# Optimization experiments

Hardware: AMD Instinct MI355X
Metric: run time of the kernel (lower is better)

## Reference

```python
import jax, jax.numpy as jnp
import numpy as np

RADIUS = 5.0
NB = 50                      # num_basis = radius * basis_density_per_A
SN, VN = 16, 8               # node irreps: 16x0e + 8x1o
SO, VO = 8, 4                # out  irreps:  8x0e + 4x1o
H = 128                      # MLP hidden width
NUMEL1 = SN*SN + SN*VN + VN*VN + VN*SN            # 576  (uvw paths, sh muls = 1)
NUMEL2 = SN*SN*SO + SN*VN*VO + VN*SN*VO + VN*VN*SO  # 3584
N_NODES, N_EDGES = 10000, 50000
SQ3 = 3.0 ** 0.5

# normalize2mom constant for silu (e3nn normalizes act so E[act(z)^2]=1, z~N(0,1))
_z = np.linspace(-10.0, 10.0, 40001)
_dz = _z[1] - _z[0]
_phi = np.exp(-0.5 * _z**2) / np.sqrt(2.0 * np.pi)
_s = _z / (1.0 + np.exp(-_z))
ACT_C = float(1.0 / np.sqrt(np.sum(_s * _s * _phi) * _dz))


def _mlp(x, w1, w2):
    # e3nn FullyConnectedNet: variance-preserving layers, normalized act on hidden
    h = ACT_C * jax.nn.silu(x @ (w1 / np.sqrt(w1.shape[0])))
    return h @ (w2 / np.sqrt(w2.shape[0]))


def _soft_one_hot(d):
    # soft_one_hot_linspace(basis='smooth_finite', cutoff=True)
    step = RADIUS / (NB + 1)
    values = jnp.linspace(0.0, RADIUS, NB + 2)[1:-1]
    diff = (d[:, None] - values) / step
    def sus(t):
        return jnp.where(t > 0.0, jnp.exp(-1.0 / jnp.where(t > 0.0, t, 1.0)), 0.0)
    return 1.14136 * np.exp(2.0) * sus(diff + 1.0) * sus(1.0 - diff)


def setup_inputs() -> dict:
    key = jax.random.key(0)
    ks = jax.random.split(key, 7)
    return {
        "edge_index": jax.random.randint(ks[0], (2, N_EDGES), 0, N_NODES),
        "pos": 1.5 * jax.random.normal(ks[1], (N_NODES, 3), jnp.float32),
        "x": jax.random.normal(ks[2], (N_NODES, SN + 3 * VN), jnp.float32),
        "lig_w1": jax.random.normal(ks[3], (NB, H), jnp.float32),
        "lig_w2": jax.random.normal(ks[4], (H, NUMEL1), jnp.float32),
        "rec_w1": jax.random.normal(ks[5], (NB, H), jnp.float32),
        "rec_w2": jax.random.normal(ks[6], (H, NUMEL2), jnp.float32),
    }


def reference(edge_index, pos, x, lig_w1, lig_w2, rec_w1, rec_w2):
    rec, lig = edge_index[0], edge_index[1]
    vec = pos[lig] - pos[rec]                         # [E,3]
    d = jnp.sqrt(jnp.sum(vec * vec, axis=1))
    sh1 = SQ3 * vec / jnp.maximum(d, 1e-12)[:, None]  # l=1 SH, 'component' norm; sh0 == 1
    demb = _soft_one_hot(d) * np.sqrt(NB)             # [E,NB]

    # ---- TP1: node(lig) x sh -> node, per-edge uvw weights ----
    w = _mlp(demb, lig_w1, lig_w2)                    # [E,576]
    o = 0
    W000 = w[:, o:o + SN * SN].reshape(-1, SN, SN); o += SN * SN
    W011 = w[:, o:o + SN * VN].reshape(-1, SN, VN); o += SN * VN
    W101 = w[:, o:o + VN * VN].reshape(-1, VN, VN); o += VN * VN
    W110 = w[:, o:o + VN * SN].reshape(-1, VN, SN)
    xl = x[lig]
    s1 = xl[:, :SN]
    v1 = xl[:, SN:].reshape(-1, VN, 3)
    c0 = (1.0 / (SN + VN)) ** 0.5                     # path norm, out 0e
    c1 = (3.0 / (SN + VN)) ** 0.5                     # path norm, out 1o
    v1_dot_sh = jnp.einsum('euk,ek->eu', v1, sh1)
    s_a = c0 * (jnp.einsum('euw,eu->ew', W000, s1)
                + jnp.einsum('euw,eu->ew', W110, v1_dot_sh) / SQ3)
    v_a = (c1 / SQ3) * (jnp.einsum('euw,eu,ek->ewk', W011, s1, sh1)
                        + jnp.einsum('euw,euk->ewk', W101, v1))

    # ---- TP2: msg x node(rec) -> out, per-edge uvw weights ----
    w = _mlp(demb, rec_w1, rec_w2)                    # [E,3584]
    o = 0
    W000 = w[:, o:o + SN * SN * SO].reshape(-1, SN, SN, SO); o += SN * SN * SO
    W011 = w[:, o:o + SN * VN * VO].reshape(-1, SN, VN, VO); o += SN * VN * VO
    W101 = w[:, o:o + VN * SN * VO].reshape(-1, VN, SN, VO); o += VN * SN * VO
    W110 = w[:, o:o + VN * VN * SO].reshape(-1, VN, VN, SO)
    xr = x[rec]
    s_b = xr[:, :SN]
    v_b = xr[:, SN:].reshape(-1, VN, 3)
    c0 = (1.0 / (SN * SN + VN * VN)) ** 0.5
    c1 = (3.0 / (SN * VN + VN * SN)) ** 0.5
    s_out = c0 * (jnp.einsum('euvw,eu,ev->ew', W000, s_a, s_b)
                  + jnp.einsum('euvw,euk,evk->ew', W110, v_a, v_b) / SQ3)
    v_out = (c1 / SQ3) * (jnp.einsum('euvw,eu,evk->ewk', W011, s_a, v_b)
                          + jnp.einsum('euvw,euk,ev->ewk', W101, v_a, s_b))
    return jnp.concatenate([s_out, v_out.reshape(-1, VO * 3)], axis=1)  # [E, 20]
```

## Files before the change

### kernel.cpp

```cpp
#include <hip/hip_runtime.h>
#include <math.h>

#define NE     50000
#define NNODE  10000
#define HDIM   128
#define GBIN   2048
#define NLUT   2049
#define NC     4160
#define NC1    576
#define NCHMAX 3611
#define MPAD   2064
#define NB_W2T 1040
#define NB_EDGE 196

typedef _Float16 h2 __attribute__((ext_vector_type(2)));
typedef _Float16 h8 __attribute__((ext_vector_type(8)));
typedef float f32x4 __attribute__((ext_vector_type(4)));

typedef __fp16 hp2 __attribute__((ext_vector_type(2)));
typedef __fp16 hp4 __attribute__((ext_vector_type(4)));
typedef __fp16 hp8 __attribute__((ext_vector_type(8)));

static __device__ __forceinline__ float fdot2f(hp2 p, hp2 q, float acc) {
  return __builtin_amdgcn_fdot2(p, q, acc, false);
}
static __device__ __forceinline__ hp2 pk2(float a, float b) {
  hp2 r = __builtin_amdgcn_cvt_pkrtz(a, b);
  return r;
}
static __device__ __forceinline__ hp2 mkh2(__fp16 a, __fp16 b) {
  hp2 o; o[0] = a; o[1] = b;
  return o;
}

#define SQ3C        1.7320508075688772f
#define INV_SQ3     0.5773502691896258f
#define C0_1F       0.20412414523193154f
#define C1_1_OS3F   0.20412414523193154f
#define C0_2F       0.05590169943749474f
#define C1_2_OS3F   0.0625f
#define INV_SQRT_H  0.08838834764831845f
#define DELTA       (5.0f/2048.0f)
#define INV_DELTA   409.6f
#define STEP_INV    (51.0f/5.0f)

__global__ __launch_bounds__(256) void k_fused(
    const float* __restrict__ lw1, const float* __restrict__ rw1,
    const float* __restrict__ lw2, const float* __restrict__ rw2,
    const float actc, const float K0C,
    _Float16* __restrict__ Hl, _Float16* __restrict__ Hr,
    _Float16* __restrict__ w2t,
    const int* __restrict__ ei, const float* __restrict__ pos,
    float* __restrict__ out, int* __restrict__ bin_e,
    float* __restrict__ f_e, int* __restrict__ cnt) {
  const int bid = blockIdx.x;
  const int tid = threadIdx.x;
  if (bid < MPAD) {
    const int g = bid;
    const int which = tid >> 7, hc = tid & 127;
    const float* __restrict__ w1 = which ? rw1 : lw1;
    float h = 0.f;
    if (g <= GBIN) {
      const float tt = (float)g * DELTA * STEP_INV;
      const int i0 = (int)floorf(tt);
      float z = 0.f;
#pragma unroll
      for (int k = 0; k < 2; ++k) {
        const int ii = i0 + k;
        if (ii >= 1 && ii <= 50) {
          const float diff = tt - (float)ii;
          const float a = diff + 1.f, b = 1.f - diff;
          if (a > 0.f && b > 0.f) {
            const float val = K0C * __expf(-1.f / a - 1.f / b);
            z += val * w1[(ii - 1) * HDIM + hc];
          }
        }
      }
      h = actc * z / (1.f + __expf(-z)) * INV_SQRT_H;
    }
    _Float16* __restrict__ H = which ? Hr : Hl;
    H[(size_t)g * HDIM + hc] = (_Float16)h;
  } else if (bid < MPAD + NB_W2T) {
    const int gid = (bid - MPAD) * 256 + tid;
    const int k2 = gid / NC;
    const int n  = gid - k2 * NC;
    float a, b;
    if (n < NC1) {
      a = lw2[(size_t)(2 * k2) * NC1 + n];
      b = lw2[(size_t)(2 * k2 + 1) * NC1 + n];
    } else {
      const int m = n - NC1;
      a = rw2[(size_t)(2 * k2) * 3584 + m];
      b = rw2[(size_t)(2 * k2 + 1) * 3584 + m];
    }
    h2 p; p[0] = (_Float16)a; p[1] = (_Float16)b;
    *(h2*)(w2t + (size_t)n * HDIM + 2 * k2) = p;
  } else {
    const int e = (bid - MPAD - NB_W2T) * 256 + tid;
    if (e >= NE) return;
    const int rec = ei[e], lig = ei[NE + e];
    const float ax = pos[lig * 3 + 0] - pos[rec * 3 + 0];
    const float ay = pos[lig * 3 + 1] - pos[rec * 3 + 1];
    const float az = pos[lig * 3 + 2] - pos[rec * 3 + 2];
    const float d = sqrtf(ax * ax + ay * ay + az * az);
    if (d > 0.f && d < 5.0f) {
      const float tf = d * INV_DELTA;
      int b = (int)tf;
      if (b > GBIN - 1) b = GBIN - 1;
      bin_e[e] = b;
      f_e[e] = tf - (float)b;
      atomicAdd(&cnt[b], 1);
    } else {
      bin_e[e] = -1;
      float* o = out + (size_t)e * 20;
#pragma unroll
      for (int i2 = 0; i2 < 20; ++i2) o[i2] = 0.f;
    }
  }
}

__global__ __launch_bounds__(256) void k_lutm(
    const _Float16* __restrict__ Hl, const _Float16* __restrict__ Hr,
    const _Float16* __restrict__ w2t, _Float16* __restrict__ lut) {
  const int tid = threadIdx.x;
  const int nt = blockIdx.y * 4 + (tid >> 6);
  const int mt = blockIdx.x;
  const int l  = tid & 63;
  const int rc = l & 15;
  const int kg = (l >> 4) * 8;
  const _Float16* __restrict__ Ap =
      ((nt < 36) ? Hl : Hr) + (size_t)(mt * 16 + rc) * HDIM + kg;
  const _Float16* __restrict__ Bp = w2t + (size_t)(nt * 16 + rc) * HDIM + kg;
  f32x4 acc = {0.f, 0.f, 0.f, 0.f};
#pragma unroll
  for (int kc = 0; kc < 4; ++kc) {
    h8 a = *(const h8*)(Ap + kc * 32);
    h8 b = *(const h8*)(Bp + kc * 32);
    acc = __builtin_amdgcn_mfma_f32_16x16x32_f16(a, b, acc, 0, 0, 0);
  }
#pragma unroll
  for (int r = 0; r < 4; ++r) {
    const int g = mt * 16 + (l >> 4) * 4 + r;
    if (g <= GBIN) lut[(size_t)g * NC + nt * 16 + rc] = (_Float16)acc[r];
  }
}

__global__ void k_scan(const int* __restrict__ cnt, int* __restrict__ offs,
                       int* __restrict__ woff, int* __restrict__ chunk_bin,
                       int* __restrict__ chunk_start, int* __restrict__ nch) {
  __shared__ int lds[256];
  const int t = threadIdx.x;
  int loc[8];
  int s = 0;
#pragma unroll
  for (int i = 0; i < 8; ++i) { loc[i] = cnt[t * 8 + i]; s += loc[i]; }
  lds[t] = s;
  __syncthreads();
  for (int o = 1; o < 256; o <<= 1) {
    int v = 0;
    if (t >= o) v = lds[t - o];
    __syncthreads();
    lds[t] += v;
    __syncthreads();
  }
  int run = lds[t] - s;
  int runs[8];
#pragma unroll
  for (int i = 0; i < 8; ++i) {
    runs[i] = run;
    offs[t * 8 + i] = run;
    woff[t * 8 + i] = run;
    run += loc[i];
  }
  if (t == 255) offs[GBIN] = run;

  int ccnt[8];
  int csum = 0;
#pragma unroll
  for (int i = 0; i < 8; ++i) { ccnt[i] = (loc[i] + 31) >> 5; csum += ccnt[i]; }
  __syncthreads();
  lds[t] = csum;
  __syncthreads();
  for (int o = 1; o < 256; o <<= 1) {
    int v = 0;
    if (t >= o) v = lds[t - o];
    __syncthreads();
    lds[t] += v;
    __syncthreads();
  }
  int crun = lds[t] - csum;
#pragma unroll
  for (int i = 0; i < 8; ++i) {
    for (int c = 0; c < ccnt[i]; ++c) {
      chunk_bin[crun]   = t * 8 + i;
      chunk_start[crun] = runs[i] + c * 32;
      ++crun;
    }
  }
  if (t == 255) nch[0] = lds[255];
}

__global__ void k_scatter(const int* __restrict__ bin_e, int* __restrict__ woff,
                          int* __restrict__ sorted) {
  const int e = blockIdx.x * 256 + threadIdx.x;
  if (e >= NE) return;
  const int b = bin_e[e];
  if (b >= 0) {
    const int p = atomicAdd(&woff[b], 1);
    sorted[p] = e;
  }
}

__global__ __launch_bounds__(128) void k_epi(
    const _Float16* __restrict__ lut, const int* __restrict__ chunk_bin,
    const int* __restrict__ chunk_start, const int* __restrict__ offs,
    const int* __restrict__ sorted, const float* __restrict__ f_e,
    const int* __restrict__ ei, const float* __restrict__ pos,
    const float* __restrict__ x, float* __restrict__ out,
    const int* __restrict__ nch) {
  __shared__ __fp16 WP[2 * NC];
  const int bid = blockIdx.x;
  if (bid >= nch[0]) return;
  const int b     = chunk_bin[bid];
  const int start = chunk_start[bid];
  const int end0  = offs[b + 1];
  const int end   = (start + 32 < end0) ? (start + 32) : end0;
  const int tid = threadIdx.x;
  {
    const hp8* r0 = (const hp8*)(lut + (size_t)b * NC);
    const hp8* r1 = (const hp8*)(lut + (size_t)(b + 1) * NC);
    hp8* dst = (hp8*)WP;
    for (int i = tid; i < NC / 8; i += 128) {
      hp8 a = r0[i], c = r1[i];
      dst[2 * i]     = __builtin_shufflevector(a, c, 0, 8, 1, 9, 2, 10, 3, 11);
      dst[2 * i + 1] = __builtin_shufflevector(a, c, 4, 12, 5, 13, 6, 14, 7, 15);
    }
  }
  __syncthreads();
  const int s  = tid & 3;
  const int qb = (tid & 63) & ~3;
  const int slot = start + (tid >> 2);
  if (slot >= end) return;

  const int e = sorted[slot];
  const float f = f_e[e];
  const float fm = 1.f - f;
  const int rec = ei[e], lig = ei[NE + e];
  const float ax = pos[lig * 3 + 0] - pos[rec * 3 + 0];
  const float ay = pos[lig * 3 + 1] - pos[rec * 3 + 1];
  const float az = pos[lig * 3 + 2] - pos[rec * 3 + 2];
  const float d = sqrtf(ax * ax + ay * ay + az * az);
  const float inv = SQ3C / fmaxf(d, 1e-12f);
  const float sh0 = ax * inv, sh1 = ay * inv, sh2 = az * inv;

  float s1[16], v1[24];
  {
    const float4* xl = (const float4*)(x + (size_t)lig * 40);
#pragma unroll
    for (int j = 0; j < 4; ++j) {
      float4 v = xl[j];
      s1[j * 4 + 0] = v.x; s1[j * 4 + 1] = v.y; s1[j * 4 + 2] = v.z; s1[j * 4 + 3] = v.w;
    }
#pragma unroll
    for (int j = 0; j < 6; ++j) {
      float4 v = xl[4 + j];
      v1[j * 4 + 0] = v.x; v1[j * 4 + 1] = v.y; v1[j * 4 + 2] = v.z; v1[j * 4 + 3] = v.w;
    }
  }
  float vs[8];
#pragma unroll
  for (int u = 0; u < 8; ++u)
    vs[u] = (v1[u * 3] * sh0 + v1[u * 3 + 1] * sh1 + v1[u * 3 + 2] * sh2) * INV_SQ3;

  float A[4] = {0.f, 0.f, 0.f, 0.f};
#pragma unroll
  for (int u = 0; u < 16; ++u) {
    hp8 w = *(const hp8*)(WP + 2 * (u * 16 + s * 4));
    hp2 sp = pk2(s1[u] * fm, s1[u] * f);
    A[0] = fdot2f(mkh2(w[0], w[1]), sp, A[0]);
    A[1] = fdot2f(mkh2(w[2], w[3]), sp, A[1]);
    A[2] = fdot2f(mkh2(w[4], w[5]), sp, A[2]);
    A[3] = fdot2f(mkh2(w[6], w[7]), sp, A[3]);
  }
#pragma unroll
  for (int u = 0; u < 8; ++u) {
    hp8 w = *(const hp8*)(WP + 2 * (448 + u * 16 + s * 4));
    hp2 sp = pk2(vs[u] * fm, vs[u] * f);
    A[0] = fdot2f(mkh2(w[0], w[1]), sp, A[0]);
    A[1] = fdot2f(mkh2(w[2], w[3]), sp, A[1]);
    A[2] = fdot2f(mkh2(w[4], w[5]), sp, A[2]);
    A[3] = fdot2f(mkh2(w[6], w[7]), sp, A[3]);
  }
  const float sa0 = C0_1F * A[0];
  const float sa1 = C0_1F * A[1];
  const float sa2 = C0_1F * A[2];
  const float sa3 = C0_1F * A[3];

  float vaA0, vaA1, vaA2, vaB0, vaB1, vaB2;
  {
    float cA = 0.f, cB = 0.f;
#pragma unroll
    for (int u = 0; u < 16; ++u) {
      hp4 w = *(const hp4*)(WP + 2 * (256 + u * 8 + s * 2));
      hp2 sp = pk2(s1[u] * fm, s1[u] * f);
      cA = fdot2f(mkh2(w[0], w[1]), sp, cA);
      cB = fdot2f(mkh2(w[2], w[3]), sp, cB);
    }
    float tAx = 0.f, tAy = 0.f, tAz = 0.f, tBx = 0.f, tBy = 0.f, tBz = 0.f;
#pragma unroll
    for (int u = 0; u < 8; ++u) {
      hp4 w = *(const hp4*)(WP + 2 * (384 + u * 8 + s * 2));
      hp2 px = pk2(v1[u * 3] * fm,     v1[u * 3] * f);
      hp2 py = pk2(v1[u * 3 + 1] * fm, v1[u * 3 + 1] * f);
      hp2 pz = pk2(v1[u * 3 + 2] * fm, v1[u * 3 + 2] * f);
      hp2 pa = mkh2(w[0], w[1]);
      hp2 pb = mkh2(w[2], w[3]);
      tAx = fdot2f(pa, px, tAx); tAy = fdot2f(pa, py, tAy); tAz = fdot2f(pa, pz, tAz);
      tBx = fdot2f(pb, px, tBx); tBy = fdot2f(pb, py, tBy); tBz = fdot2f(pb, pz, tBz);
    }
    vaA0 = C1_1_OS3F * (cA * sh0 + tAx);
    vaA1 = C1_1_OS3F * (cA * sh1 + tAy);
    vaA2 = C1_1_OS3F * (cA * sh2 + tAz);
    vaB0 = C1_1_OS3F * (cB * sh0 + tBx);
    vaB1 = C1_1_OS3F * (cB * sh1 + tBy);
    vaB2 = C1_1_OS3F * (cB * sh2 + tBz);
  }

  float saF[16];
#pragma unroll
  for (int k = 0; k < 16; ++k) {
    const float v = ((k & 3) == 0) ? sa0 : ((k & 3) == 1) ? sa1 : ((k & 3) == 2) ? sa2 : sa3;
    saF[k] = __shfl(v, qb + (k >> 2), 64);
  }
  float vaF[24];
#pragma unroll
  for (int w = 0; w < 8; ++w) {
    const int src = qb + (w >> 1);
    const float x0 = (w & 1) ? vaB0 : vaA0;
    const float x1 = (w & 1) ? vaB1 : vaA1;
    const float x2 = (w & 1) ? vaB2 : vaA2;
    vaF[w * 3 + 0] = __shfl(x0, src, 64);
    vaF[w * 3 + 1] = __shfl(x1, src, 64);
    vaF[w * 3 + 2] = __shfl(x2, src, 64);
  }

  const float* xr = x + (size_t)rec * 40;
  const float sbl0 = xr[s],      sbl1 = xr[4 + s];
  const float sbl2 = xr[8 + s],  sbl3 = xr[12 + s];
  const float vbA0 = xr[16 + s * 3 + 0], vbA1 = xr[16 + s * 3 + 1], vbA2 = xr[16 + s * 3 + 2];
  const float vbB0 = xr[16 + (s + 4) * 3 + 0], vbB1 = xr[16 + (s + 4) * 3 + 1], vbB2 = xr[16 + (s + 4) * 3 + 2];

  float oe[20];

  {
    float so[8];
#pragma unroll
    for (int w = 0; w < 8; ++w) so[w] = 0.f;
#pragma unroll
    for (int u = 0; u < 16; ++u) {
      const float su = saF[u];
      const __fp16* rp = WP + 2 * (576 + u * 128 + s * 8);
#pragma unroll
      for (int vv = 0; vv < 4; ++vv) {
        const float q = su * ((vv == 0) ? sbl0 : (vv == 1) ? sbl1 : (vv == 2) ? sbl2 : sbl3);
        hp2 qp = pk2(q * fm, q * f);
        hp8 wa = *(const hp8*)(rp + 2 * (vv * 32));
        hp8 wb = *(const hp8*)(rp + 2 * (vv * 32) + 8);
        so[0] = fdot2f(mkh2(wa[0], wa[1]), qp, so[0]);
        so[1] = fdot2f(mkh2(wa[2], wa[3]), qp, so[1]);
        so[2] = fdot2f(mkh2(wa[4], wa[5]), qp, so[2]);
        so[3] = fdot2f(mkh2(wa[6], wa[7]), qp, so[3]);
        so[4] = fdot2f(mkh2(wb[0], wb[1]), qp, so[4]);
        so[5] = fdot2f(mkh2(wb[2], wb[3]), qp, so[5]);
        so[6] = fdot2f(mkh2(wb[4], wb[5]), qp, so[6]);
        so[7] = fdot2f(mkh2(wb[6], wb[7]), qp, so[7]);
      }
    }
#pragma unroll
    for (int u = 0; u < 8; ++u) {
      const float a0 = vaF[u * 3], a1 = vaF[u * 3 + 1], a2 = vaF[u * 3 + 2];
      const __fp16* rp = WP + 2 * (3648 + u * 64 + s * 8);
#pragma unroll
      for (int vv = 0; vv < 2; ++vv) {
        const float b0v = vv ? vbB0 : vbA0;
        const float b1v = vv ? vbB1 : vbA1;
        const float b2v = vv ? vbB2 : vbA2;
        const float dd = (a0 * b0v + a1 * b1v + a2 * b2v) * INV_SQ3;
        hp2 qp = pk2(dd * fm, dd * f);
        hp8 wa = *(const hp8*)(rp + 2 * (vv * 32));
        hp8 wb = *(const hp8*)(rp + 2 * (vv * 32) + 8);
        so[0] = fdot2f(mkh2(wa[0], wa[1]), qp, so[0]);
        so[1] = fdot2f(mkh2(wa[2], wa[3]), qp, so[1]);
        so[2] = fdot2f(mkh2(wa[4], wa[5]), qp, so[2]);
        so[3] = fdot2f(mkh2(wa[6], wa[7]), qp, so[3]);
        so[4] = fdot2f(mkh2(wb[0], wb[1]), qp, so[4]);
        so[5] = fdot2f(mkh2(wb[2], wb[3]), qp, so[5]);
        so[6] = fdot2f(mkh2(wb[4], wb[5]), qp, so[6]);
        so[7] = fdot2f(mkh2(wb[6], wb[7]), qp, so[7]);
      }
    }
#pragma unroll
    for (int w = 0; w < 8; ++w) oe[w] = C0_2F * so[w];
  }

  {
    float uo[12];
#pragma unroll
    for (int w = 0; w < 12; ++w) uo[w] = 0.f;
#pragma unroll
    for (int u = 0; u < 16; ++u) {
      const float su = saF[u];
      const __fp16* rp = WP + 2 * (2624 + u * 32 + s * 4);
#pragma unroll
      for (int vv = 0; vv < 2; ++vv) {
        const float q0 = su * (vv ? vbB0 : vbA0);
        const float q1 = su * (vv ? vbB1 : vbA1);
        const float q2 = su * (vv ? vbB2 : vbA2);
        hp2 q0p = pk2(q0 * fm, q0 * f);
        hp2 q1p = pk2(q1 * fm, q1 * f);
        hp2 q2p = pk2(q2 * fm, q2 * f);
        hp8 w = *(const hp8*)(rp + 2 * (vv * 16));
        hp2 p0 = mkh2(w[0], w[1]);
        hp2 p1 = mkh2(w[2], w[3]);
        hp2 p2 = mkh2(w[4], w[5]);
        hp2 p3 = mkh2(w[6], w[7]);
        uo[0] = fdot2f(p0, q0p, uo[0]); uo[1]  = fdot2f(p0, q1p, uo[1]);  uo[2]  = fdot2f(p0, q2p, uo[2]);
        uo[3] = fdot2f(p1, q0p, uo[3]); uo[4]  = fdot2f(p1, q1p, uo[4]);  uo[5]  = fdot2f(p1, q2p, uo[5]);
        uo[6] = fdot2f(p2, q0p, uo[6]); uo[7]  = fdot2f(p2, q1p, uo[7]);  uo[8]  = fdot2f(p2, q2p, uo[8]);
        uo[9] = fdot2f(p3, q0p, uo[9]); uo[10] = fdot2f(p3, q1p, uo[10]); uo[11] = fdot2f(p3, q2p, uo[11]);
      }
    }
#pragma unroll
    for (int u = 0; u < 8; ++u) {
      const float a0 = vaF[u * 3], a1 = vaF[u * 3 + 1], a2 = vaF[u * 3 + 2];
      const __fp16* rp = WP + 2 * (3136 + u * 64 + s * 4);
#pragma unroll
      for (int vv = 0; vv < 4; ++vv) {
        const float sbv = (vv == 0) ? sbl0 : (vv == 1) ? sbl1 : (vv == 2) ? sbl2 : sbl3;
        const float q0 = a0 * sbv, q1 = a1 * sbv, q2 = a2 * sbv;
        hp2 q0p = pk2(q0 * fm, q0 * f);
        hp2 q1p = pk2(q1 * fm, q1 * f);
        hp2 q2p = pk2(q2 * fm, q2 * f);
        hp8 w = *(const hp8*)(rp + 2 * (vv * 16));
        hp2 p0 = mkh2(w[0], w[1]);
        hp2 p1 = mkh2(w[2], w[3]);
        hp2 p2 = mkh2(w[4], w[5]);
        hp2 p3 = mkh2(w[6], w[7]);
        uo[0] = fdot2f(p0, q0p, uo[0]); uo[1]  = fdot2f(p0, q1p, uo[1]);  uo[2]  = fdot2f(p0, q2p, uo[2]);
        uo[3] = fdot2f(p1, q0p, uo[3]); uo[4]  = fdot2f(p1, q1p, uo[4]);  uo[5]  = fdot2f(p1, q2p, uo[5]);
        uo[6] = fdot2f(p2, q0p, uo[6]); uo[7]  = fdot2f(p2, q1p, uo[7]);  uo[8]  = fdot2f(p2, q2p, uo[8]);
        uo[9] = fdot2f(p3, q0p, uo[9]); uo[10] = fdot2f(p3, q1p, uo[10]); uo[11] = fdot2f(p3, q2p, uo[11]);
      }
    }
#pragma unroll
    for (int w = 0; w < 12; ++w) oe[8 + w] = C1_2_OS3F * uo[w];
  }

#pragma unroll
  for (int w = 0; w < 20; ++w) {
    oe[w] += __shfl_xor(oe[w], 1, 64);
    oe[w] += __shfl_xor(oe[w], 2, 64);
  }
  if (s == 0) {
    float4* op = (float4*)(out + (size_t)e * 20);
#pragma unroll
    for (int j = 0; j < 5; ++j) {
      float4 o4;
      o4.x = oe[j * 4 + 0]; o4.y = oe[j * 4 + 1];
      o4.z = oe[j * 4 + 2]; o4.w = oe[j * 4 + 3];
      op[j] = o4;
    }
  }
}

extern "C" void kernel_launch(void* const* d_in, const int* in_sizes, int n_in,
                              void* d_out, int out_size, void* d_ws, size_t ws_size,
                              hipStream_t stream) {
  const int*   ei  = (const int*)d_in[0];
  const float* pos = (const float*)d_in[1];
  const float* x   = (const float*)d_in[2];
  const float* lw1 = (const float*)d_in[3];
  const float* lw2 = (const float*)d_in[4];
  const float* rw1 = (const float*)d_in[5];
  const float* rw2 = (const float*)d_in[6];
  float* out = (float*)d_out;
  char*  ws  = (char*)d_ws;

  size_t o = 0;
  _Float16* lut = (_Float16*)(ws + o); o += (size_t)NLUT * NC * 2;
  o = (o + 15) & ~(size_t)15;
  _Float16* Hl  = (_Float16*)(ws + o); o += (size_t)MPAD * HDIM * 2;
  _Float16* Hr  = (_Float16*)(ws + o); o += (size_t)MPAD * HDIM * 2;
  _Float16* w2t = (_Float16*)(ws + o); o += (size_t)NC * HDIM * 2;
  o = (o + 15) & ~(size_t)15;
  int*   bin_e = (int*)(ws + o);  o += (size_t)NE * 4;
  float* f_e   = (float*)(ws + o); o += (size_t)NE * 4;
  int*   cnt   = (int*)(ws + o);  o += (size_t)GBIN * 4;
  int*   offs  = (int*)(ws + o);  o += (size_t)(GBIN + 1) * 4 + 12;
  int*   woff  = (int*)(ws + o);  o += (size_t)GBIN * 4;
  int*   sorted = (int*)(ws + o); o += (size_t)NE * 4;
  int*   chunk_bin   = (int*)(ws + o); o += (size_t)NCHMAX * 4;
  int*   chunk_start = (int*)(ws + o); o += (size_t)NCHMAX * 4;
  int*   nch = (int*)(ws + o); o += 16;

  double ssum = 0.0;
  const double dz = 20.0 / 40000.0;
  for (int i = 0; i <= 40000; ++i) {
    const double z = -10.0 + dz * (double)i;
    const double sil = z / (1.0 + exp(-z));
    const double phi = exp(-0.5 * z * z) / sqrt(2.0 * M_PI);
    ssum += sil * sil * phi;
  }
  const float actc = (float)(1.0 / sqrt(ssum * dz));
  const float k0c  = (float)(1.14136 * exp(2.0));

  hipMemsetAsync(cnt, 0, GBIN * 4, stream);
  k_fused<<<MPAD + NB_W2T + NB_EDGE, 256, 0, stream>>>(
      lw1, rw1, lw2, rw2, actc, k0c, Hl, Hr, w2t, ei, pos, out, bin_e, f_e, cnt);
  k_lutm<<<dim3(129, 65), 256, 0, stream>>>(Hl, Hr, w2t, lut);
  k_scan<<<1, 256, 0, stream>>>(cnt, offs, woff, chunk_bin, chunk_start, nch);
  k_scatter<<<(NE + 255) / 256, 256, 0, stream>>>(bin_e, woff, sorted);
  k_epi<<<NCHMAX, 128, 0, stream>>>(lut, chunk_bin, chunk_start, offs, sorted, f_e,
                                    ei, pos, x, out, nch);
}
```

Measured before the change: 107.0 us.

## Store LUT pre-interleaved by adjacent bins and fold scan into GEMM launch

The LUT GEMM now writes each value twice into an interleaved layout that pairs bin g with bin g+1. The epilogue can then fill its shared-memory table with a straight vector copy instead of loading two rows and shuffling them. The single-block scan kernel becomes one extra block of the GEMM grid, which removes a launch. In exchange the LUT roughly doubles in size, the GEMM writes scattered 2-byte strided stores, and the scan block is serialized inside a large grid.

```diff
diff --git a/kernel.cpp b/kernel.cpp
--- a/kernel.cpp
+++ b/kernel.cpp
@@ -5,13 +5,13 @@
 #define NNODE  10000
 #define HDIM   128
 #define GBIN   2048
-#define NLUT   2049
 #define NC     4160
 #define NC1    576
 #define NCHMAX 3611
 #define MPAD   2064
 #define NB_W2T 1040
 #define NB_EDGE 196
+#define NB_GEMM (129*65)
 
 typedef _Float16 h2 __attribute__((ext_vector_type(2)));
 typedef _Float16 h8 __attribute__((ext_vector_type(8)));
@@ -121,83 +121,90 @@
 
 __global__ __launch_bounds__(256) void k_lutm(
     const _Float16* __restrict__ Hl, const _Float16* __restrict__ Hr,
-    const _Float16* __restrict__ w2t, _Float16* __restrict__ lut) {
+    const _Float16* __restrict__ w2t, __fp16* __restrict__ ilut,
+    const int* __restrict__ cnt, int* __restrict__ offs,
+    int* __restrict__ woff, int* __restrict__ chunk_bin,
+    int* __restrict__ chunk_start, int* __restrict__ nch) {
+  const int bid = blockIdx.x;
   const int tid = threadIdx.x;
-  const int nt = blockIdx.y * 4 + (tid >> 6);
-  const int mt = blockIdx.x;
-  const int l  = tid & 63;
-  const int rc = l & 15;
-  const int kg = (l >> 4) * 8;
-  const _Float16* __restrict__ Ap =
-      ((nt < 36) ? Hl : Hr) + (size_t)(mt * 16 + rc) * HDIM + kg;
-  const _Float16* __restrict__ Bp = w2t + (size_t)(nt * 16 + rc) * HDIM + kg;
-  f32x4 acc = {0.f, 0.f, 0.f, 0.f};
-#pragma unroll
-  for (int kc = 0; kc < 4; ++kc) {
-    h8 a = *(const h8*)(Ap + kc * 32);
-    h8 b = *(const h8*)(Bp + kc * 32);
-    acc = __builtin_amdgcn_mfma_f32_16x16x32_f16(a, b, acc, 0, 0, 0);
-  }
-#pragma unroll
-  for (int r = 0; r < 4; ++r) {
-    const int g = mt * 16 + (l >> 4) * 4 + r;
-    if (g <= GBIN) lut[(size_t)g * NC + nt * 16 + rc] = (_Float16)acc[r];
-  }
-}
-
-__global__ void k_scan(const int* __restrict__ cnt, int* __restrict__ offs,
-                       int* __restrict__ woff, int* __restrict__ chunk_bin,
-                       int* __restrict__ chunk_start, int* __restrict__ nch) {
-  __shared__ int lds[256];
-  const int t = threadIdx.x;
-  int loc[8];
-  int s = 0;
-#pragma unroll
-  for (int i = 0; i < 8; ++i) { loc[i] = cnt[t * 8 + i]; s += loc[i]; }
-  lds[t] = s;
-  __syncthreads();
-  for (int o = 1; o < 256; o <<= 1) {
-    int v = 0;
-    if (t >= o) v = lds[t - o];
+  if (bid < NB_GEMM) {
+    const int mt = bid % 129;
+    const int nt = (bid / 129) * 4 + (tid >> 6);
+    const int l  = tid & 63;
+    const int rc = l & 15;
+    const int kg = (l >> 4) * 8;
+    const _Float16* __restrict__ Ap =
+        ((nt < 36) ? Hl : Hr) + (size_t)(mt * 16 + rc) * HDIM + kg;
+    const _Float16* __restrict__ Bp = w2t + (size_t)(nt * 16 + rc) * HDIM + kg;
+    f32x4 acc = {0.f, 0.f, 0.f, 0.f};
+#pragma unroll
+    for (int kc = 0; kc < 4; ++kc) {
+      h8 a = *(const h8*)(Ap + kc * 32);
+      h8 b = *(const h8*)(Bp + kc * 32);
+      acc = __builtin_amdgcn_mfma_f32_16x16x32_f16(a, b, acc, 0, 0, 0);
+    }
+    const int n = nt * 16 + rc;
+#pragma unroll
+    for (int r = 0; r < 4; ++r) {
+      const int g = mt * 16 + (l >> 4) * 4 + r;
+      if (g <= GBIN) {
+        const __fp16 v = (__fp16)acc[r];
+        if (g < GBIN) ilut[(size_t)g * (2 * NC) + 2 * n] = v;
+        if (g >= 1)   ilut[(size_t)(g - 1) * (2 * NC) + 2 * n + 1] = v;
+      }
+    }
+  } else {
+    __shared__ int lds[256];
+    const int t = tid;
+    int loc[8];
+    int s = 0;
+#pragma unroll
+    for (int i = 0; i < 8; ++i) { loc[i] = cnt[t * 8 + i]; s += loc[i]; }
+    lds[t] = s;
     __syncthreads();
-    lds[t] += v;
+    for (int o = 1; o < 256; o <<= 1) {
+      int v = 0;
+      if (t >= o) v = lds[t - o];
+      __syncthreads();
+      lds[t] += v;
+      __syncthreads();
+    }
+    int run = lds[t] - s;
+    int runs[8];
+#pragma unroll
+    for (int i = 0; i < 8; ++i) {
+      runs[i] = run;
+      offs[t * 8 + i] = run;
+      woff[t * 8 + i] = run;
+      run += loc[i];
+    }
+    if (t == 255) offs[GBIN] = run;
+
+    int ccnt[8];
+    int csum = 0;
+#pragma unroll
+    for (int i = 0; i < 8; ++i) { ccnt[i] = (loc[i] + 31) >> 5; csum += ccnt[i]; }
     __syncthreads();
-  }
-  int run = lds[t] - s;
-  int runs[8];
-#pragma unroll
-  for (int i = 0; i < 8; ++i) {
-    runs[i] = run;
-    offs[t * 8 + i] = run;
-    woff[t * 8 + i] = run;
-    run += loc[i];
-  }
-  if (t == 255) offs[GBIN] = run;
-
-  int ccnt[8];
-  int csum = 0;
-#pragma unroll
-  for (int i = 0; i < 8; ++i) { ccnt[i] = (loc[i] + 31) >> 5; csum += ccnt[i]; }
-  __syncthreads();
-  lds[t] = csum;
-  __syncthreads();
-  for (int o = 1; o < 256; o <<= 1) {
-    int v = 0;
-    if (t >= o) v = lds[t - o];
+    lds[t] = csum;
     __syncthreads();
-    lds[t] += v;
-    __syncthreads();
-  }
-  int crun = lds[t] - csum;
-#pragma unroll
-  for (int i = 0; i < 8; ++i) {
-    for (int c = 0; c < ccnt[i]; ++c) {
-      chunk_bin[crun]   = t * 8 + i;
-      chunk_start[crun] = runs[i] + c * 32;
-      ++crun;
-    }
-  }
-  if (t == 255) nch[0] = lds[255];
+    for (int o = 1; o < 256; o <<= 1) {
+      int v = 0;
+      if (t >= o) v = lds[t - o];
+      __syncthreads();
+      lds[t] += v;
+      __syncthreads();
+    }
+    int crun = lds[t] - csum;
+#pragma unroll
+    for (int i = 0; i < 8; ++i) {
+      for (int c = 0; c < ccnt[i]; ++c) {
+        chunk_bin[crun]   = t * 8 + i;
+        chunk_start[crun] = runs[i] + c * 32;
+        ++crun;
+      }
+    }
+    if (t == 255) nch[0] = lds[255];
+  }
 }
 
 __global__ void k_scatter(const int* __restrict__ bin_e, int* __restrict__ woff,
@@ -212,7 +219,7 @@
 }
 
 __global__ __launch_bounds__(128) void k_epi(
-    const _Float16* __restrict__ lut, const int* __restrict__ chunk_bin,
+    const __fp16* __restrict__ ilut, const int* __restrict__ chunk_bin,
     const int* __restrict__ chunk_start, const int* __restrict__ offs,
     const int* __restrict__ sorted, const float* __restrict__ f_e,
     const int* __restrict__ ei, const float* __restrict__ pos,
@@ -227,14 +234,9 @@
   const int end   = (start + 32 < end0) ? (start + 32) : end0;
   const int tid = threadIdx.x;
   {
-    const hp8* r0 = (const hp8*)(lut + (size_t)b * NC);
-    const hp8* r1 = (const hp8*)(lut + (size_t)(b + 1) * NC);
-    hp8* dst = (hp8*)WP;
-    for (int i = tid; i < NC / 8; i += 128) {
-      hp8 a = r0[i], c = r1[i];
-      dst[2 * i]     = __builtin_shufflevector(a, c, 0, 8, 1, 9, 2, 10, 3, 11);
-      dst[2 * i + 1] = __builtin_shufflevector(a, c, 4, 12, 5, 13, 6, 14, 7, 15);
-    }
+    const uint4* src = (const uint4*)(ilut + (size_t)b * (2 * NC));
+    uint4* dst = (uint4*)WP;
+    for (int i = tid; i < 1040; i += 128) dst[i] = src[i];
   }
   __syncthreads();
   const int s  = tid & 3;
@@ -487,7 +489,7 @@
   char*  ws  = (char*)d_ws;
 
   size_t o = 0;
-  _Float16* lut = (_Float16*)(ws + o); o += (size_t)NLUT * NC * 2;
+  __fp16* ilut = (__fp16*)(ws + o); o += (size_t)GBIN * (2 * NC) * 2;
   o = (o + 15) & ~(size_t)15;
   _Float16* Hl  = (_Float16*)(ws + o); o += (size_t)MPAD * HDIM * 2;
   _Float16* Hr  = (_Float16*)(ws + o); o += (size_t)MPAD * HDIM * 2;
@@ -517,9 +519,9 @@
   hipMemsetAsync(cnt, 0, GBIN * 4, stream);
   k_fused<<<MPAD + NB_W2T + NB_EDGE, 256, 0, stream>>>(
       lw1, rw1, lw2, rw2, actc, k0c, Hl, Hr, w2t, ei, pos, out, bin_e, f_e, cnt);
-  k_lutm<<<dim3(129, 65), 256, 0, stream>>>(Hl, Hr, w2t, lut);
-  k_scan<<<1, 256, 0, stream>>>(cnt, offs, woff, chunk_bin, chunk_start, nch);
+  k_lutm<<<NB_GEMM + 1, 256, 0, stream>>>(Hl, Hr, w2t, ilut, cnt, offs, woff,
+                                          chunk_bin, chunk_start, nch);
   k_scatter<<<(NE + 255) / 256, 256, 0, stream>>>(bin_e, woff, sorted);
-  k_epi<<<NCHMAX, 128, 0, stream>>>(lut, chunk_bin, chunk_start, offs, sorted, f_e,
+  k_epi<<<NCHMAX, 128, 0, stream>>>(ilut, chunk_bin, chunk_start, offs, sorted, f_e,
                                     ei, pos, x, out, nch);
 }
```

After: 104.9 us. -2.0%, faster.
